# Performance work log

Measured on AMD Instinct MI355X. Metric: run time of the kernel, lower is better.

## Reference

```python
import jax, jax.numpy as jnp
import numpy as np

HIDDEN = 1024
HEADS = 16
HEAD_DIM = HIDDEN // HEADS


def setup_inputs() -> dict:
    key = jax.random.key(0)
    ks = jax.random.split(key, 12)
    B, S = 2, 2048
    scale = 1.0 / np.sqrt(HIDDEN)
    inp = {
        "query": jax.random.normal(ks[0], (B, S, HIDDEN), dtype=jnp.float32),
        "key": jax.random.normal(ks[1], (B, S, HIDDEN), dtype=jnp.float32),
        "value": jax.random.normal(ks[2], (B, S, HIDDEN), dtype=jnp.float32),
        "mask": jax.random.randint(ks[3], (B, 1, 1, S), 0, 2, dtype=jnp.int32),
        "Wq": jax.random.normal(ks[4], (HIDDEN, HIDDEN), dtype=jnp.float32) * scale,
        "bq": jnp.zeros((HIDDEN,), dtype=jnp.float32),
        "Wk": jax.random.normal(ks[5], (HIDDEN, HIDDEN), dtype=jnp.float32) * scale,
        "bk": jnp.zeros((HIDDEN,), dtype=jnp.float32),
        "Wv": jax.random.normal(ks[6], (HIDDEN, HIDDEN), dtype=jnp.float32) * scale,
        "bv": jnp.zeros((HIDDEN,), dtype=jnp.float32),
        "Wo": jax.random.normal(ks[7], (HIDDEN, HIDDEN), dtype=jnp.float32) * scale,
        "bo": jnp.zeros((HIDDEN,), dtype=jnp.float32),
    }
    return inp


def reference(query, key, value, mask, Wq, bq, Wk, bk, Wv, bv, Wo, bo):
    B, S, _ = query.shape
    # linear projections (x @ W + b), split heads -> [B, H, S, Dh]
    def split_heads(x):
        return x.reshape(B, -1, HEADS, HEAD_DIM).transpose(0, 2, 1, 3)

    q = split_heads(query @ Wq + bq)
    k = split_heads(key @ Wk + bk)
    v = split_heads(value @ Wv + bv)

    # scaled dot-product attention, full [B,H,S,S] scores as in original
    scores = jnp.einsum("bhqd,bhkd->bhqk", q, k) / np.sqrt(HEAD_DIM)
    scores = jnp.where(mask == 0, jnp.float32(-1e9), scores)
    weights = jax.nn.softmax(scores, axis=-1)
    x = jnp.einsum("bhqk,bhkd->bhqd", weights, v)

    # merge heads -> [B, S, hidden], output projection, then transpose(1,2)
    x = x.transpose(0, 2, 1, 3).reshape(B, -1, HIDDEN)
    out = (x @ Wo + bo).transpose(0, 2, 1)  # [B, hidden, S]
    return out
```

## Files before the change

### kernel.cpp

```cpp
#include <hip/hip_runtime.h>


typedef unsigned short ushort_t;
typedef unsigned long long ull_t;
typedef __attribute__((ext_vector_type(8))) short short8;
typedef __attribute__((ext_vector_type(4))) float f32x4;

#define S_LEN 2048
#define HID 1024
#define NH 16
#define MTOT 4096
#define KB 128
#define PERHEAD 131072
#define QSCALE 0.18033688011112042f

__device__ __forceinline__ void bsplit(float x, ushort_t& h, ushort_t& l) {
  unsigned u = __float_as_uint(x);
  unsigned hr = (u + 0x7fffu + ((u >> 16) & 1u)) >> 16;
  h = (ushort_t)hr;
  float hf = __uint_as_float(hr << 16);
  float r = x - hf;
  unsigned u2 = __float_as_uint(r);
  l = (ushort_t)((u2 + 0x7fffu + ((u2 >> 16) & 1u)) >> 16);
}

__device__ __forceinline__ void qsplit4(float v0, float v1, float v2, float v3,
                                        ull_t& hi, ull_t& lo) {
  unsigned u0 = __float_as_uint(v0), u1 = __float_as_uint(v1);
  unsigned u2 = __float_as_uint(v2), u3 = __float_as_uint(v3);
  unsigned h01 = (u0 >> 16) | (u1 & 0xffff0000u);
  unsigned h23 = (u2 >> 16) | (u3 & 0xffff0000u);
  float r0 = v0 - __uint_as_float(u0 & 0xffff0000u);
  float r1 = v1 - __uint_as_float(u1 & 0xffff0000u);
  float r2 = v2 - __uint_as_float(u2 & 0xffff0000u);
  float r3 = v3 - __uint_as_float(u3 & 0xffff0000u);
  unsigned l01, l23;
  asm("v_cvt_pk_bf16_f32 %0, %1, %2" : "=v"(l01) : "v"(r0), "v"(r1));
  asm("v_cvt_pk_bf16_f32 %0, %1, %2" : "=v"(l23) : "v"(r2), "v"(r3));
  hi = (ull_t)h01 | ((ull_t)h23 << 32);
  lo = (ull_t)l01 | ((ull_t)l23 << 32);
}

__device__ __forceinline__ void gload16(const ushort_t* g, ushort_t* l) {
  __builtin_amdgcn_global_load_lds(
      (const __attribute__((address_space(1))) unsigned int*)g,
      (__attribute__((address_space(3))) unsigned int*)l, 16, 0, 0);
}

__global__ __launch_bounds__(256) void pack_mat(const float* __restrict__ src,
                                                ushort_t* __restrict__ hi,
                                                ushort_t* __restrict__ lo,
                                                int bmode) {
  int tid = blockIdx.x * 256 + threadIdx.x;
  int r = tid & 15;
  int k8 = (tid >> 4) & (KB - 1);
  int o16 = tid >> 11;
  float v[8];
  if (bmode == 0) {
    const float* s = src + (size_t)(o16 * 16 + r) * HID + k8 * 8;
    const f32x4 f0 = *(const f32x4*)s;
    const f32x4 f1 = *(const f32x4*)(s + 4);
#pragma unroll
    for (int j = 0; j < 4; ++j) { v[j] = f0[j]; v[4 + j] = f1[j]; }
  } else {
#pragma unroll
    for (int j = 0; j < 8; ++j)
      v[j] = src[(size_t)(k8 * 8 + j) * HID + o16 * 16 + r];
  }
  short8 H, L;
#pragma unroll
  for (int j = 0; j < 8; ++j) {
    ushort_t h, l;
    bsplit(v[j], h, l);
    H[j] = (short)h;
    L[j] = (short)l;
  }
  *(short8*)(hi + (size_t)tid * 8) = H;
  *(short8*)(lo + (size_t)tid * 8) = L;
}

__global__ __launch_bounds__(256) void mask_to_float(const int* __restrict__ m,
                                                     float* __restrict__ mf) {
  int i = blockIdx.x * 256 + threadIdx.x;
  mf[i] = m[i] ? 0.f : -1e9f;
}

__global__ __launch_bounds__(256) void gemm_pack(
    const ushort_t* __restrict__ Ahi, const ushort_t* __restrict__ Alo,
    const ushort_t* __restrict__ Bhi, const ushort_t* __restrict__ Blo,
    const float* __restrict__ bias, ushort_t* __restrict__ Ohi,
    ushort_t* __restrict__ Olo, float* __restrict__ Ofp, float scale,
    int mode) {
  __shared__ ushort_t sbuf[16384];
  const int m0 = blockIdx.y * 128;
  const int n0 = blockIdx.x * 64;
  const int lane = threadIdx.x & 63;
  const int wv = threadIdx.x >> 6;
  const int wr = wv >> 1, wc = wv & 1;
  const int l15 = lane & 15, l4 = lane >> 4;

  f32x4 acc[4][2] = {};

  const ushort_t* gsrc[6];
  ushort_t* ldst[6];
  {
    const size_t ab = (size_t)(m0 >> 4) * 16384 + lane * 8;
    const size_t bb = (size_t)(n0 >> 4) * 16384 + lane * 8;
#pragma unroll
    for (int t = 0; t < 6; ++t) {
      int c = t * 4 + wv;
      if (c < 8) {
        gsrc[t] = Ahi + ab + (size_t)c * 16384;
        ldst[t] = &sbuf[c * 512];
      } else if (c < 16) {
        gsrc[t] = Alo + ab + (size_t)(c - 8) * 16384;
        ldst[t] = &sbuf[4096 + (c - 8) * 512];
      } else if (c < 20) {
        gsrc[t] = Bhi + bb + (size_t)(c - 16) * 16384;
        ldst[t] = &sbuf[8192 + (c - 16) * 512];
      } else {
        gsrc[t] = Blo + bb + (size_t)(c - 20) * 16384;
        ldst[t] = &sbuf[10240 + (c - 20) * 512];
      }
    }
  }

  for (int ks = 0; ks < HID / 32; ++ks) {
    __syncthreads();
#pragma unroll
    for (int t = 0; t < 6; ++t) gload16(gsrc[t] + ks * 512, ldst[t]);
    asm volatile("s_waitcnt vmcnt(0)" ::: "memory");
    __syncthreads();

    short8 ah[4], al[4], bh[2], bl[2];
#pragma unroll
    for (int mi = 0; mi < 4; ++mi) {
      int e = (wr * 4 + mi) * 512 + l4 * 128 + l15 * 8;
      ah[mi] = *(const short8*)&sbuf[e];
      al[mi] = *(const short8*)&sbuf[4096 + e];
    }
#pragma unroll
    for (int ni = 0; ni < 2; ++ni) {
      int e = (wc * 2 + ni) * 512 + l4 * 128 + l15 * 8;
      bh[ni] = *(const short8*)&sbuf[8192 + e];
      bl[ni] = *(const short8*)&sbuf[10240 + e];
    }
#pragma unroll
    for (int mi = 0; mi < 4; ++mi)
#pragma unroll
      for (int ni = 0; ni < 2; ++ni) {
        acc[mi][ni] = __builtin_amdgcn_mfma_f32_16x16x32_bf16(al[mi], bh[ni], acc[mi][ni], 0, 0, 0);
        acc[mi][ni] = __builtin_amdgcn_mfma_f32_16x16x32_bf16(ah[mi], bl[ni], acc[mi][ni], 0, 0, 0);
        acc[mi][ni] = __builtin_amdgcn_mfma_f32_16x16x32_bf16(ah[mi], bh[ni], acc[mi][ni], 0, 0, 0);
      }
  }

  if (mode < 2) {
    __syncthreads();
#pragma unroll
    for (int mi = 0; mi < 4; ++mi)
#pragma unroll
      for (int ni = 0; ni < 2; ++ni) {
        int col = wc * 32 + ni * 16 + l15;
        float bvv = bias[n0 + col];
#pragma unroll
        for (int i = 0; i < 4; ++i) {
          int row = wr * 64 + mi * 16 + l4 * 4 + i;
          float v = (acc[mi][ni][i] + bvv) * scale;
          ushort_t hh, ll;
          bsplit(v, hh, ll);
          int loc = (mode == 0)
                        ? (((row >> 4) * 8 + (col >> 3)) * 128 + (row & 15) * 8 + (col & 7))
                        : (((col >> 4) * 16 + (row >> 3)) * 128 + (col & 15) * 8 + (row & 7));
          sbuf[loc] = hh;
          sbuf[8192 + loc] = ll;
        }
      }
    __syncthreads();
    const int hd = n0 >> 6;
    const int b_ = m0 >> 11;
    const int s0 = m0 & (S_LEN - 1);
    const size_t hb = (size_t)(b_ * NH + hd) * PERHEAD;
#pragma unroll
    for (int r2 = 0; r2 < 2; ++r2) {
      int t = r2 * 256 + threadIdx.x;
      size_t dst;
      if (mode == 0) {
        int m16loc = (t * 16) >> 10, rem = (t * 16) & 1023;
        dst = hb + (size_t)((s0 >> 4) + m16loc) * 1024 + rem;
      } else {
        int dg = (t * 16) >> 11, rem = (t * 16) & 2047;
        dst = hb + (size_t)dg * 32768 + (size_t)(s0 >> 3) * 128 + rem;
      }
      *(short8*)(Ohi + dst) = *(const short8*)&sbuf[t * 16];
      *(short8*)(Ohi + dst + 8) = *(const short8*)&sbuf[t * 16 + 8];
      *(short8*)(Olo + dst) = *(const short8*)&sbuf[8192 + t * 16];
      *(short8*)(Olo + dst + 8) = *(const short8*)&sbuf[8192 + t * 16 + 8];
    }
  } else {
#pragma unroll
    for (int mi = 0; mi < 4; ++mi)
#pragma unroll
      for (int ni = 0; ni < 2; ++ni) {
        int col = n0 + wc * 32 + ni * 16 + l15;
        float bvv = bias[col];
        int m = m0 + wr * 64 + mi * 16 + l4 * 4;
        int b_ = m >> 11, s = m & (S_LEN - 1);
        f32x4 v = acc[mi][ni];
        v[0] += bvv; v[1] += bvv; v[2] += bvv; v[3] += bvv;
        *(f32x4*)(Ofp + (size_t)(b_ * HID + col) * S_LEN + s) = v;
      }
  }
}

__global__ __launch_bounds__(256) void attn_kernel(
    const ushort_t* __restrict__ Qhi, const ushort_t* __restrict__ Qlo,
    const ushort_t* __restrict__ Khi, const ushort_t* __restrict__ Klo,
    const ushort_t* __restrict__ Vhi, const ushort_t* __restrict__ Vlo,
    const float* __restrict__ maskF, ushort_t* __restrict__ Xhi,
    ushort_t* __restrict__ Xlo) {
  __shared__ ushort_t KtH[4096], KtL[4096], VtH[4096], VtL[4096];
  __shared__ ushort_t PH[4][2][1024], PL[4][2][1024];
  const int qb = blockIdx.x, h = blockIdx.y, b = blockIdx.z;
  const int lane = threadIdx.x & 63, wv = threadIdx.x >> 6;
  const int l15 = lane & 15, l4 = lane >> 4;
  const size_t hb = (size_t)(b * NH + h) * PERHEAD;

  short8 qh[2][2], ql[2][2];
#pragma unroll
  for (int qi = 0; qi < 2; ++qi)
#pragma unroll
    for (int kk = 0; kk < 2; ++kk) {
      size_t o = hb + (size_t)(qb * 8 + wv * 2 + qi) * 1024 + (kk * 4 + l4) * 128 + l15 * 8;
      qh[qi][kk] = *(const short8*)(Qhi + o);
      ql[qi][kk] = *(const short8*)(Qlo + o);
    }

  const float* mrow = maskF + b * S_LEN;
  f32x4 o_acc[2][4] = {};
  float m_r[2] = {-1e30f, -1e30f}, l_r[2] = {0.f, 0.f};

  for (int kt = 0; kt < S_LEN / 64; ++kt) {
    __syncthreads();
#pragma unroll
    for (int c = 0; c < 2; ++c) {
      int chunk = wv * 2 + c;
      size_t ko = hb + (size_t)kt * 4096 + chunk * 512 + lane * 8;
      gload16(Khi + ko, &KtH[chunk * 512]);
      gload16(Klo + ko, &KtL[chunk * 512]);
      int dg = chunk >> 1, hf = chunk & 1;
      size_t vo = hb + (size_t)dg * 32768 + (size_t)kt * 1024 + hf * 512 + lane * 8;
      gload16(Vhi + vo, &VtH[chunk * 512]);
      gload16(Vlo + vo, &VtL[chunk * 512]);
    }
    f32x4 mf[4];
#pragma unroll
    for (int cg = 0; cg < 4; ++cg)
      mf[cg] = *(const f32x4*)(mrow + kt * 64 + cg * 16 + l4 * 4);
    asm volatile("s_waitcnt vmcnt(0)" ::: "memory");
    __syncthreads();

    f32x4 sc[2][4];
#pragma unroll
    for (int cg = 0; cg < 4; ++cg) {
      short8 kh[2], kl[2];
#pragma unroll
      for (int kk = 0; kk < 2; ++kk) {
        int e = cg * 1024 + (kk * 4 + l4) * 128 + l15 * 8;
        kh[kk] = *(const short8*)&KtH[e];
        kl[kk] = *(const short8*)&KtL[e];
      }
#pragma unroll
      for (int qi = 0; qi < 2; ++qi) {
        f32x4 a = {};
#pragma unroll
        for (int kk = 0; kk < 2; ++kk) {
          a = __builtin_amdgcn_mfma_f32_16x16x32_bf16(kl[kk], qh[qi][kk], a, 0, 0, 0);
          a = __builtin_amdgcn_mfma_f32_16x16x32_bf16(kh[kk], ql[qi][kk], a, 0, 0, 0);
          a = __builtin_amdgcn_mfma_f32_16x16x32_bf16(kh[kk], qh[qi][kk], a, 0, 0, 0);
        }
        a[0] += mf[cg][0]; a[1] += mf[cg][1]; a[2] += mf[cg][2]; a[3] += mf[cg][3];
        sc[qi][cg] = a;
      }
    }

#pragma unroll
    for (int qi = 0; qi < 2; ++qi) {
      float tm = fmaxf(fmaxf(fmaxf(sc[qi][0][0], sc[qi][0][1]), fmaxf(sc[qi][0][2], sc[qi][0][3])),
                       fmaxf(fmaxf(sc[qi][1][0], sc[qi][1][1]), fmaxf(sc[qi][1][2], sc[qi][1][3])));
      float tm2 = fmaxf(fmaxf(fmaxf(sc[qi][2][0], sc[qi][2][1]), fmaxf(sc[qi][2][2], sc[qi][2][3])),
                        fmaxf(fmaxf(sc[qi][3][0], sc[qi][3][1]), fmaxf(sc[qi][3][2], sc[qi][3][3])));
      tm = fmaxf(tm, tm2);
      tm = fmaxf(tm, __shfl_xor(tm, 16));
      tm = fmaxf(tm, __shfl_xor(tm, 32));
      float mn;
      if (__all(tm <= m_r[qi])) {
        mn = m_r[qi];
      } else {
        mn = fmaxf(m_r[qi], tm);
        float fs = exp2f(m_r[qi] - mn);
        m_r[qi] = mn;
        l_r[qi] *= fs;
#pragma unroll
        for (int dg = 0; dg < 4; ++dg) o_acc[qi][dg] *= fs;
      }
      float ts = 0.f;
#pragma unroll
      for (int cg = 0; cg < 4; ++cg) {
        float p0 = exp2f(sc[qi][cg][0] - mn);
        float p1 = exp2f(sc[qi][cg][1] - mn);
        float p2 = exp2f(sc[qi][cg][2] - mn);
        float p3 = exp2f(sc[qi][cg][3] - mn);
        ts += (p0 + p1) + (p2 + p3);
        ull_t hi, lo;
        qsplit4(p0, p1, p2, p3, hi, lo);
        int e = (cg * 2 + (l4 >> 1)) * 128 + l15 * 8 + (l4 & 1) * 4;
        *(ull_t*)&PH[wv][qi][e] = hi;
        *(ull_t*)&PL[wv][qi][e] = lo;
      }
      ts += __shfl_xor(ts, 16);
      ts += __shfl_xor(ts, 32);
      l_r[qi] += ts;
    }

#pragma unroll
    for (int kk = 0; kk < 2; ++kk) {
      short8 vh[4], vl[4];
#pragma unroll
      for (int dg = 0; dg < 4; ++dg) {
        int e = dg * 1024 + (kk * 4 + l4) * 128 + l15 * 8;
        vh[dg] = *(const short8*)&VtH[e];
        vl[dg] = *(const short8*)&VtL[e];
      }
#pragma unroll
      for (int qi = 0; qi < 2; ++qi) {
        int pe = (kk * 4 + l4) * 128 + l15 * 8;
        short8 pbh = *(const short8*)&PH[wv][qi][pe];
        short8 pbl = *(const short8*)&PL[wv][qi][pe];
#pragma unroll
        for (int dg = 0; dg < 4; ++dg) {
          o_acc[qi][dg] = __builtin_amdgcn_mfma_f32_16x16x32_bf16(vh[dg], pbl, o_acc[qi][dg], 0, 0, 0);
          o_acc[qi][dg] = __builtin_amdgcn_mfma_f32_16x16x32_bf16(vl[dg], pbh, o_acc[qi][dg], 0, 0, 0);
          o_acc[qi][dg] = __builtin_amdgcn_mfma_f32_16x16x32_bf16(vh[dg], pbh, o_acc[qi][dg], 0, 0, 0);
        }
      }
    }
  }

#pragma unroll
  for (int qi = 0; qi < 2; ++qi) {
    float rl = 1.0f / l_r[qi];
    int m16 = b * 128 + qb * 8 + wv * 2 + qi;
#pragma unroll
    for (int dg = 0; dg < 4; ++dg) {
      float v0 = o_acc[qi][dg][0] * rl;
      float v1 = o_acc[qi][dg][1] * rl;
      float v2 = o_acc[qi][dg][2] * rl;
      float v3 = o_acc[qi][dg][3] * rl;
      ull_t hi, lo;
      qsplit4(v0, v1, v2, v3, hi, lo);
      size_t dst = (size_t)m16 * 16384 + (size_t)(h * 8 + dg * 2 + (l4 >> 1)) * 128 + l15 * 8 + (l4 & 1) * 4;
      *(ull_t*)(Xhi + dst) = hi;
      *(ull_t*)(Xlo + dst) = lo;
    }
  }
}

extern "C" void kernel_launch(void* const* d_in, const int* in_sizes, int n_in,
                              void* d_out, int out_size, void* d_ws,
                              size_t ws_size, hipStream_t stream) {
  (void)in_sizes; (void)n_in; (void)out_size; (void)ws_size;
  const float* query = (const float*)d_in[0];
  const float* key = (const float*)d_in[1];
  const float* value = (const float*)d_in[2];
  const int* mask = (const int*)d_in[3];
  const float* Wq = (const float*)d_in[4];
  const float* bq = (const float*)d_in[5];
  const float* Wk = (const float*)d_in[6];
  const float* bk = (const float*)d_in[7];
  const float* Wv = (const float*)d_in[8];
  const float* bv = (const float*)d_in[9];
  const float* Wo = (const float*)d_in[10];
  const float* bo = (const float*)d_in[11];
  float* out = (float*)d_out;

  const size_t EL = (size_t)MTOT * HID;
  const size_t WEL = (size_t)HID * HID;
  ushort_t* p = (ushort_t*)d_ws;
  ushort_t* X0h = p;            ushort_t* X0l = X0h + EL;
  ushort_t* X1h = X0l + EL;     ushort_t* X1l = X1h + EL;
  ushort_t* X2h = X1l + EL;     ushort_t* X2l = X2h + EL;
  ushort_t* W0h = X2l + EL;     ushort_t* W0l = W0h + WEL;
  ushort_t* W1h = W0l + WEL;    ushort_t* W1l = W1h + WEL;
  ushort_t* W2h = W1l + WEL;    ushort_t* W2l = W2h + WEL;
  ushort_t* W3h = W2l + WEL;    ushort_t* W3l = W3h + WEL;
  ushort_t* Qh = W3l + WEL;     ushort_t* Ql = Qh + EL;
  float* maskF = (float*)W0h;

  pack_mat<<<dim3(2048), dim3(256), 0, stream>>>(query, X0h, X0l, 0);
  pack_mat<<<dim3(2048), dim3(256), 0, stream>>>(key, X1h, X1l, 0);
  pack_mat<<<dim3(2048), dim3(256), 0, stream>>>(value, X2h, X2l, 0);
  pack_mat<<<dim3(512), dim3(256), 0, stream>>>(Wq, W0h, W0l, 1);
  pack_mat<<<dim3(512), dim3(256), 0, stream>>>(Wk, W1h, W1l, 1);
  pack_mat<<<dim3(512), dim3(256), 0, stream>>>(Wv, W2h, W2l, 1);
  pack_mat<<<dim3(512), dim3(256), 0, stream>>>(Wo, W3h, W3l, 1);

  dim3 gg(HID / 64, MTOT / 128);
  gemm_pack<<<gg, 256, 0, stream>>>(X0h, X0l, W0h, W0l, bq, Qh, Ql, nullptr,
                                    QSCALE, 0);
  mask_to_float<<<dim3(16), dim3(256), 0, stream>>>(mask, maskF);
  gemm_pack<<<gg, 256, 0, stream>>>(X1h, X1l, W1h, W1l, bk, X0h, X0l, nullptr,
                                    1.0f, 0);
  gemm_pack<<<gg, 256, 0, stream>>>(X2h, X2l, W2h, W2l, bv, X1h, X1l, nullptr,
                                    1.0f, 1);

  attn_kernel<<<dim3(S_LEN / 128, NH, 2), 256, 0, stream>>>(
      Qh, Ql, X0h, X0l, X1h, X1l, maskF, X2h, X2l);

  gemm_pack<<<gg, 256, 0, stream>>>(X2h, X2l, W3h, W3l, bo, nullptr, nullptr,
                                    out, 1.0f, 2);
}
```

Measured before the change: 405.5 us.

## Double-buffer LDS tiles in projection GEMM to overlap loads with MFMA

Grows the shared buffer to two stages and issues global-to-LDS loads for the next K slice before computing on the current one, with one wait and barrier per iteration instead of two. This hides global load latency behind the MFMA work. LDS use per block rises from 32KB to 48KB, which may lower occupancy.

```diff
diff --git a/kernel.cpp b/kernel.cpp
--- a/kernel.cpp
+++ b/kernel.cpp
@@ -91,7 +91,7 @@
     const float* __restrict__ bias, ushort_t* __restrict__ Ohi,
     ushort_t* __restrict__ Olo, float* __restrict__ Ofp, float scale,
     int mode) {
-  __shared__ ushort_t sbuf[16384];
+  __shared__ ushort_t sbuf[24576];
   const int m0 = blockIdx.y * 128;
   const int n0 = blockIdx.x * 64;
   const int lane = threadIdx.x & 63;
@@ -102,7 +102,7 @@
   f32x4 acc[4][2] = {};
 
   const ushort_t* gsrc[6];
-  ushort_t* ldst[6];
+  int loff[6];
   {
     const size_t ab = (size_t)(m0 >> 4) * 16384 + lane * 8;
     const size_t bb = (size_t)(n0 >> 4) * 16384 + lane * 8;
@@ -111,39 +111,46 @@
       int c = t * 4 + wv;
       if (c < 8) {
         gsrc[t] = Ahi + ab + (size_t)c * 16384;
-        ldst[t] = &sbuf[c * 512];
+        loff[t] = c * 512;
       } else if (c < 16) {
         gsrc[t] = Alo + ab + (size_t)(c - 8) * 16384;
-        ldst[t] = &sbuf[4096 + (c - 8) * 512];
+        loff[t] = 4096 + (c - 8) * 512;
       } else if (c < 20) {
         gsrc[t] = Bhi + bb + (size_t)(c - 16) * 16384;
-        ldst[t] = &sbuf[8192 + (c - 16) * 512];
+        loff[t] = 8192 + (c - 16) * 512;
       } else {
         gsrc[t] = Blo + bb + (size_t)(c - 20) * 16384;
-        ldst[t] = &sbuf[10240 + (c - 20) * 512];
-      }
-    }
-  }
-
+        loff[t] = 10240 + (c - 20) * 512;
+      }
+    }
+  }
+
+#pragma unroll
+  for (int t = 0; t < 6; ++t) gload16(gsrc[t], &sbuf[loff[t]]);
+  asm volatile("s_waitcnt vmcnt(0)" ::: "memory");
+  __syncthreads();
+
+  int cur = 0;
   for (int ks = 0; ks < HID / 32; ++ks) {
-    __syncthreads();
-#pragma unroll
-    for (int t = 0; t < 6; ++t) gload16(gsrc[t] + ks * 512, ldst[t]);
-    asm volatile("s_waitcnt vmcnt(0)" ::: "memory");
-    __syncthreads();
+    if (ks < HID / 32 - 1) {
+#pragma unroll
+      for (int t = 0; t < 6; ++t)
+        gload16(gsrc[t] + (ks + 1) * 512, &sbuf[(cur ^ 1) * 12288 + loff[t]]);
+    }
+    const ushort_t* sb = &sbuf[cur * 12288];
 
     short8 ah[4], al[4], bh[2], bl[2];
 #pragma unroll
     for (int mi = 0; mi < 4; ++mi) {
       int e = (wr * 4 + mi) * 512 + l4 * 128 + l15 * 8;
-      ah[mi] = *(const short8*)&sbuf[e];
-      al[mi] = *(const short8*)&sbuf[4096 + e];
+      ah[mi] = *(const short8*)&sb[e];
+      al[mi] = *(const short8*)&sb[4096 + e];
     }
 #pragma unroll
     for (int ni = 0; ni < 2; ++ni) {
       int e = (wc * 2 + ni) * 512 + l4 * 128 + l15 * 8;
-      bh[ni] = *(const short8*)&sbuf[8192 + e];
-      bl[ni] = *(const short8*)&sbuf[10240 + e];
+      bh[ni] = *(const short8*)&sb[8192 + e];
+      bl[ni] = *(const short8*)&sb[10240 + e];
     }
 #pragma unroll
     for (int mi = 0; mi < 4; ++mi)
@@ -153,10 +160,12 @@
         acc[mi][ni] = __builtin_amdgcn_mfma_f32_16x16x32_bf16(ah[mi], bl[ni], acc[mi][ni], 0, 0, 0);
         acc[mi][ni] = __builtin_amdgcn_mfma_f32_16x16x32_bf16(ah[mi], bh[ni], acc[mi][ni], 0, 0, 0);
       }
+    asm volatile("s_waitcnt vmcnt(0)" ::: "memory");
+    __syncthreads();
+    cur ^= 1;
   }
 
   if (mode < 2) {
-    __syncthreads();
 #pragma unroll
     for (int mi = 0; mi < 4; ++mi)
 #pragma unroll
```

Result: no change. 402.5 us (-0.7%).
